# Kernel optimization log

Measured on AMD Instinct MI355X. Metric: run time of the kernel, lower is better.

The kernel has to match this reference:

```python
import jax, jax.numpy as jnp
import numpy as np

# dims: B batch, T frames, N tokens/frame, C embed, H heads, D=C//H, MEM memory slots
B, T, N, C = 8, 16, 196, 768
H = 8
D = C // H
MEM = 196          # mem_size; with N=196 -> _init_t = 1, M stays == MEM
HID = 4 * C        # mlp_ratio * embed_dim
STD = 0.02


def _mlp(x, w1, b1, w2, b2):
    # timm-style Mlp: fc1 -> GELU -> fc2 (dropout = 0)
    return jax.nn.gelu(x @ w1 + b1, approximate=False) @ w2 + b2


def _ln(x, w, b, eps=1e-5):
    mu = jnp.mean(x, axis=-1, keepdims=True)
    var = jnp.var(x, axis=-1, keepdims=True)
    return (x - mu) * jax.lax.rsqrt(var + eps) * w + b


def setup_inputs() -> dict:
    key = jax.random.key(0)
    ks = jax.random.split(key, 10)
    f32 = jnp.float32
    return {
        "cur_fea": jax.random.normal(ks[0], (B, T, N, C), f32),
        "norm1_w": jnp.ones((C,), f32), "norm1_b": jnp.zeros((C,), f32),
        "norm2_w": jnp.ones((C,), f32), "norm2_b": jnp.zeros((C,), f32),
        # c_func: Mlp(2C -> 4C -> C)
        "c_w1": jax.random.normal(ks[1], (2 * C, HID), f32) * STD, "c_b1": jnp.zeros((HID,), f32),
        "c_w2": jax.random.normal(ks[2], (HID, C), f32) * STD, "c_b2": jnp.zeros((C,), f32),
        # m_func: Mlp(C -> 4C -> C)
        "m_w1": jax.random.normal(ks[3], (C, HID), f32) * STD, "m_b1": jnp.zeros((HID,), f32),
        "m_w2": jax.random.normal(ks[4], (HID, C), f32) * STD, "m_b2": jnp.zeros((C,), f32),
        # post_func: Mlp(C -> 4C -> C)
        "p_w1": jax.random.normal(ks[5], (C, HID), f32) * STD, "p_b1": jnp.zeros((HID,), f32),
        "p_w2": jax.random.normal(ks[6], (HID, C), f32) * STD, "p_b2": jnp.zeros((C,), f32),
        # ProjectDotDistance: per-head q(c_global) . k(mem) * scale -> sigmoid
        "q_w": jax.random.normal(ks[7], (C, C), f32) * STD, "q_b": jnp.zeros((C,), f32),
        "k_w": jax.random.normal(ks[8], (C, C), f32) * STD, "k_b": jnp.zeros((C,), f32),
    }


def reference(cur_fea, norm1_w, norm1_b, norm2_w, norm2_b,
              c_w1, c_b1, c_w2, c_b2, m_w1, m_b1, m_w2, m_b2,
              p_w1, p_b1, p_w2, p_b2, q_w, q_b, k_w, k_b):
    x = _ln(cur_fea, norm1_w, norm1_b)                       # [B,T,N,C]
    # T*N > mem_size, _init_t = MEM // N = 1 -> init memory = frame 0 (no grad, torch.no_grad)
    init_mem = jax.lax.stop_gradient(x[:, 0].reshape(B, MEM, C))
    scale = D ** -0.5

    def step(mem, fea):                                      # mem [B,MEM,C], fea [B,N,C]
        ap = jnp.mean(mem, axis=1, keepdims=True)            # [B,1,C]
        cg = _mlp(jnp.concatenate([fea, jnp.broadcast_to(ap, fea.shape)], axis=-1),
                  c_w1, c_b1, c_w2, c_b2)                    # [B,N,C]
        memh = _mlp(mem, m_w1, m_b1, m_w2, m_b2).reshape(B, MEM, H, D).transpose(0, 2, 1, 3)  # [B,H,M,D]
        q = (cg @ q_w + q_b).reshape(B, N, H, D).transpose(0, 2, 1, 3)    # [B,H,N,D]
        k = (mem @ k_w + k_b).reshape(B, MEM, H, D).transpose(0, 2, 1, 3) # [B,H,M,D]
        o = jax.nn.sigmoid(jnp.einsum('bhnd,bhmd->bhnm', q, k) * scale)   # [B,H,N,M]
        cgh = cg.reshape(B, N, H, D).transpose(0, 2, 1, 3)               # [B,H,N,D]
        c = jnp.einsum('bhnm,bhnd->bmhd', o, cgh).reshape(B, MEM, C)
        c = _mlp(c, p_w1, p_b1, p_w2, p_b2)
        # mean_N((1-o) * broadcast(memh)) == mean_N(1-o) * memh (memh indep of N)
        gate = jnp.mean(1.0 - o, axis=2)                     # [B,H,M]
        og = (gate[..., None] * memh).transpose(0, 2, 1, 3).reshape(B, MEM, C)
        new_mem = _ln(c + og, norm2_w, norm2_b)
        return new_mem, None

    fea_seq = x[:, 1:].transpose(1, 0, 2, 3)                 # [T-1,B,N,C]
    final_mem, _ = jax.lax.scan(step, init_mem, fea_seq)
    return final_mem                                         # [B,MEM,C]
```

## Files before the change

### kernel.cpp

```cpp
#include <hip/hip_runtime.h>
#include <hip/hip_bf16.h>
#include <math.h>

constexpr int B_   = 8;
constexpr int T_   = 16;
constexpr int N_   = 196;
constexpr int C_   = 768;
constexpr int H_   = 8;
constexpr int D_   = 96;
constexpr int M_   = 196;
constexpr int HID_ = 3072;
constexpr int ROWS_ = B_ * N_;
constexpr int MP_   = 1664;

typedef __hip_bfloat16 bf16;
typedef __attribute__((ext_vector_type(8))) short bf16x8;
typedef __attribute__((ext_vector_type(4))) float f32x4;

__device__ __forceinline__ float b2f(bf16 x) { return __bfloat162float(x); }
__device__ __forceinline__ short bf2s(bf16 x) { union { bf16 b; short s; } u; u.b = x; return u.s; }
__device__ __forceinline__ float s2f(short x) { union { bf16 b; short s; } u; u.s = x; return __bfloat162float(u.b); }

#define GL2LDS(g, l) __builtin_amdgcn_global_load_lds( \
    (__attribute__((address_space(1))) void*)(g), \
    (__attribute__((address_space(3))) void*)(l), 16, 0, 0)

__device__ __forceinline__ void hard_barrier() {
    asm volatile("" ::: "memory");
    __builtin_amdgcn_s_barrier();
    asm volatile("" ::: "memory");
}

__device__ __forceinline__ float block_reduce_sum256(float v, float* sdata) {
    int tid = threadIdx.x;
    sdata[tid] = v;
    __syncthreads();
    for (int s = 128; s > 0; s >>= 1) {
        if (tid < s) sdata[tid] += sdata[tid + s];
        __syncthreads();
    }
    float r = sdata[0];
    __syncthreads();
    return r;
}

struct TEnt { const float* W; bf16* Wt; int K; int N; int tiles; };
struct TEnts { TEnt e[8]; };

__global__ __launch_bounds__(256) void transpose_all_kernel(TEnts tds)
{
    __shared__ float tile[32][33];
    int local = blockIdx.x;
    int i = 0;
    while (i < 7 && local >= tds.e[i].tiles) { local -= tds.e[i].tiles; ++i; }
    TEnt g = tds.e[i];
    int ntx = g.N / 32;
    int n0 = (local % ntx) * 32, k0 = (local / ntx) * 32;
    int tx = threadIdx.x & 31, ty = threadIdx.x >> 5;
#pragma unroll
    for (int r = 0; r < 32; r += 8)
        tile[ty + r][tx] = g.W[(size_t)(k0 + ty + r) * g.N + n0 + tx];
    __syncthreads();
#pragma unroll
    for (int r = 0; r < 32; r += 8)
        g.Wt[(size_t)(n0 + ty + r) * g.K + k0 + tx] = __float2bfloat16(tile[tx][ty + r]);
}

__global__ __launch_bounds__(256) void cvt_kernel(const float* __restrict__ W,
                                                  bf16* __restrict__ o, int n)
{
    int i = blockIdx.x * 256 + threadIdx.x;
    if (i < n) o[i] = __float2bfloat16(W[i]);
}

__global__ __launch_bounds__(256) void ln_frame_kernel(
    const float* __restrict__ cur, int t,
    const float* __restrict__ w, const float* __restrict__ bia,
    bf16* __restrict__ mem_bf)
{
    __shared__ float sdata[256];
    int row = blockIdx.x;
    int b = row / N_, n = row % N_;
    const float* src = cur + (((size_t)b * T_ + t) * N_ + n) * C_;
    float x[3];
    float sum = 0.f, sumsq = 0.f;
#pragma unroll
    for (int i = 0; i < 3; i++) {
        int c = threadIdx.x + i * 256;
        x[i] = src[c];
        sum += x[i]; sumsq += x[i] * x[i];
    }
    sum = block_reduce_sum256(sum, sdata);
    sumsq = block_reduce_sum256(sumsq, sdata);
    float mu = sum * (1.0f / C_);
    float var = sumsq * (1.0f / C_) - mu * mu;
    float rs = rsqrtf(var + 1e-5f);
#pragma unroll
    for (int i = 0; i < 3; i++) {
        int c = threadIdx.x + i * 256;
        mem_bf[(size_t)row * C_ + c] = __float2bfloat16((x[i] - mu) * rs * w[c] + bia[c]);
    }
}

__global__ __launch_bounds__(768) void ap_kernel(const bf16* __restrict__ mem,
                                                 float* __restrict__ ap)
{
    int b = blockIdx.x;
    int c = threadIdx.x;
    const bf16* p = mem + (size_t)b * M_ * C_ + c;
    float s = 0.f;
    for (int m = 0; m < M_; m++) s += b2f(p[(size_t)m * C_]);
    ap[b * C_ + c] = s * (1.0f / M_);
}

__global__ __launch_bounds__(256) void build_cat_kernel(
    const float* __restrict__ cur, int t,
    const float* __restrict__ w, const float* __restrict__ bia,
    const float* __restrict__ ap, bf16* __restrict__ cat)
{
    __shared__ float sdata[256];
    int row = blockIdx.x;
    int b = row / N_, n = row % N_;
    const float* src = cur + (((size_t)b * T_ + t) * N_ + n) * C_;
    float x[3];
    float sum = 0.f, sumsq = 0.f;
#pragma unroll
    for (int i = 0; i < 3; i++) {
        int c = threadIdx.x + i * 256;
        x[i] = src[c];
        sum += x[i]; sumsq += x[i] * x[i];
    }
    sum = block_reduce_sum256(sum, sdata);
    sumsq = block_reduce_sum256(sumsq, sdata);
    float mu = sum * (1.0f / C_);
    float var = sumsq * (1.0f / C_) - mu * mu;
    float rs = rsqrtf(var + 1e-5f);
    bf16* dstrow = cat + (size_t)row * (2 * C_);
#pragma unroll
    for (int i = 0; i < 3; i++) {
        int c = threadIdx.x + i * 256;
        dstrow[c] = __float2bfloat16((x[i] - mu) * rs * w[c] + bia[c]);
        dstrow[C_ + c] = __float2bfloat16(ap[b * C_ + c]);
    }
}

struct GemmDesc {
    const bf16* A; const bf16* W; const float* bias; bf16* out;
    int K; int N; int ymax; int gelu;
};
struct GemmDescs { GemmDesc d[4]; };

template <int BN>
__global__ __launch_bounds__(256) void mfma_gemm_multi(GemmDescs ds)
{
    constexpr int BM = 128;
    constexpr int TI = 4;
    constexpr int TJ = (BN / 2) / 16;
    constexpr int ABYTES = BM * 128;
    constexpr int BBYTES = BN * 128;
    constexpr int AR = ABYTES / 4096;
    constexpr int BR = BBYTES / 4096;
    constexpr int NL = AR + BR;
    __shared__ short As[2 * BM * 64];
    __shared__ short Bs[2 * BN * 64];

    GemmDesc g = ds.d[blockIdx.z];
    if ((int)blockIdx.y >= g.ymax) return;

    int tid = threadIdx.x;
    int wid = tid >> 6;
    int lane = tid & 63;
    int quad = lane >> 4, l15 = lane & 15;
    int row0 = blockIdx.x * BM;
    int col0 = blockIdx.y * BN;
    int wm = (wid >> 1) * 64;
    int wn = (wid & 1) * (BN / 2);

    f32x4 acc[TI][TJ] = {};

    const char* Ab = (const char*)g.A;
    const char* Wb = (const char*)g.W;
    const size_t Kb = (size_t)g.K * 2;
    const int base = wid * 1024;

    auto stage = [&](int k0, int sel) {
        char* Ad = (char*)As + sel * ABYTES;
        char* Bd = (char*)Bs + sel * BBYTES;
#pragma unroll
        for (int r = 0; r < AR; r++) {
            int o = r * 4096 + base + lane * 16;
            int row = o >> 7, cs = (o >> 4) & 7;
            int kc = cs ^ (row & 7);
            GL2LDS(Ab + (size_t)(row0 + row) * Kb + (size_t)k0 * 2 + kc * 16, Ad + o);
        }
#pragma unroll
        for (int r = 0; r < BR; r++) {
            int o = r * 4096 + base + lane * 16;
            int row = o >> 7, cs = (o >> 4) & 7;
            int kc = cs ^ (row & 7);
            GL2LDS(Wb + (size_t)(col0 + row) * Kb + (size_t)k0 * 2 + kc * 16, Bd + o);
        }
    };

    const int nk = g.K / 64;
    stage(0, 0);
    for (int ki = 0; ki < nk; ki++) {
        int sel = ki & 1;
        if (ki + 1 < nk) {
            stage((ki + 1) * 64, sel ^ 1);
            asm volatile("s_waitcnt vmcnt(%0)" :: "n"(NL) : "memory");
        } else {
            asm volatile("s_waitcnt vmcnt(0)" ::: "memory");
        }
        hard_barrier();
        const bf16x8* Av = (const bf16x8*)(As + sel * BM * 64);
        const bf16x8* Bv = (const bf16x8*)(Bs + sel * BN * 64);
        bf16x8 af[TI][2], bfr[TJ][2];
#pragma unroll
        for (int i = 0; i < TI; i++) {
            int r = wm + i * 16 + l15;
#pragma unroll
            for (int hh = 0; hh < 2; hh++)
                af[i][hh] = Av[r * 8 + ((hh * 4 + quad) ^ (r & 7))];
        }
#pragma unroll
        for (int j = 0; j < TJ; j++) {
            int r = wn + j * 16 + l15;
#pragma unroll
            for (int hh = 0; hh < 2; hh++)
                bfr[j][hh] = Bv[r * 8 + ((hh * 4 + quad) ^ (r & 7))];
        }
#pragma unroll
        for (int hh = 0; hh < 2; hh++)
#pragma unroll
            for (int i = 0; i < TI; i++)
#pragma unroll
                for (int j = 0; j < TJ; j++)
                    acc[i][j] = __builtin_amdgcn_mfma_f32_16x16x32_bf16(
                        af[i][hh], bfr[j][hh], acc[i][j], 0, 0, 0);
        hard_barrier();
    }

#pragma unroll
    for (int i = 0; i < TI; i++) {
        int gr = row0 + wm + i * 16 + quad * 4;
#pragma unroll
        for (int j = 0; j < TJ; j++) {
            int gc = col0 + wn + j * 16 + l15;
            float bv = g.bias ? g.bias[gc] : 0.0f;
#pragma unroll
            for (int r = 0; r < 4; r++) {
                float v = acc[i][j][r] + bv;
                if (g.gelu) v = 0.5f * v * (1.0f + erff(v * 0.7071067811865475f));
                g.out[(size_t)(gr + r) * g.N + gc] = __float2bfloat16(v);
            }
        }
    }
}

__global__ __launch_bounds__(256) void mfma_gemm_splitk(
    const bf16* __restrict__ A, const bf16* __restrict__ Wt,
    float* __restrict__ part, int K)
{
    constexpr int BM = 128;
    constexpr int BN = 64;
    constexpr int TI = 4;
    constexpr int TJ = 2;
    constexpr int ABYTES = BM * 128, BBYTES = BN * 128;
    constexpr int AR = 4, BR = 2, NL = 6;
    __shared__ short As[2 * BM * 64];
    __shared__ short Bs[2 * BN * 64];

    int tid = threadIdx.x;
    int wid = tid >> 6;
    int lane = tid & 63;
    int quad = lane >> 4, l15 = lane & 15;
    int row0 = blockIdx.x * BM;
    int col0 = blockIdx.y * BN;
    int wm = (wid >> 1) * 64;
    int wn = (wid & 1) * 32;
    int kh = K >> 1;
    int kbeg = blockIdx.z * kh;

    f32x4 acc[TI][TJ] = {};
    const char* Ab = (const char*)A;
    const char* Wb = (const char*)Wt;
    const size_t Kb = (size_t)K * 2;
    const int base = wid * 1024;

    auto stage = [&](int k0, int sel) {
        char* Ad = (char*)As + sel * ABYTES;
        char* Bd = (char*)Bs + sel * BBYTES;
#pragma unroll
        for (int r = 0; r < AR; r++) {
            int o = r * 4096 + base + lane * 16;
            int row = o >> 7, cs = (o >> 4) & 7;
            int kc = cs ^ (row & 7);
            GL2LDS(Ab + (size_t)(row0 + row) * Kb + (size_t)k0 * 2 + kc * 16, Ad + o);
        }
#pragma unroll
        for (int r = 0; r < BR; r++) {
            int o = r * 4096 + base + lane * 16;
            int row = o >> 7, cs = (o >> 4) & 7;
            int kc = cs ^ (row & 7);
            GL2LDS(Wb + (size_t)(col0 + row) * Kb + (size_t)k0 * 2 + kc * 16, Bd + o);
        }
    };

    const int nk = kh / 64;
    stage(kbeg, 0);
    for (int ki = 0; ki < nk; ki++) {
        int sel = ki & 1;
        if (ki + 1 < nk) {
            stage(kbeg + (ki + 1) * 64, sel ^ 1);
            asm volatile("s_waitcnt vmcnt(%0)" :: "n"(NL) : "memory");
        } else {
            asm volatile("s_waitcnt vmcnt(0)" ::: "memory");
        }
        hard_barrier();
        const bf16x8* Av = (const bf16x8*)(As + sel * BM * 64);
        const bf16x8* Bv = (const bf16x8*)(Bs + sel * BN * 64);
        bf16x8 af[TI][2], bfr[TJ][2];
#pragma unroll
        for (int i = 0; i < TI; i++) {
            int r = wm + i * 16 + l15;
#pragma unroll
            for (int hh = 0; hh < 2; hh++)
                af[i][hh] = Av[r * 8 + ((hh * 4 + quad) ^ (r & 7))];
        }
#pragma unroll
        for (int j = 0; j < TJ; j++) {
            int r = wn + j * 16 + l15;
#pragma unroll
            for (int hh = 0; hh < 2; hh++)
                bfr[j][hh] = Bv[r * 8 + ((hh * 4 + quad) ^ (r & 7))];
        }
#pragma unroll
        for (int hh = 0; hh < 2; hh++)
#pragma unroll
            for (int i = 0; i < TI; i++)
#pragma unroll
                for (int j = 0; j < TJ; j++)
                    acc[i][j] = __builtin_amdgcn_mfma_f32_16x16x32_bf16(
                        af[i][hh], bfr[j][hh], acc[i][j], 0, 0, 0);
        hard_barrier();
    }

    float* outp = part + (size_t)blockIdx.z * MP_ * C_;
#pragma unroll
    for (int i = 0; i < TI; i++) {
        int gr = row0 + wm + i * 16 + quad * 4;
#pragma unroll
        for (int j = 0; j < TJ; j++) {
            int gc = col0 + wn + j * 16 + l15;
#pragma unroll
            for (int r = 0; r < 4; r++)
                outp[(size_t)(gr + r) * C_ + gc] = acc[i][j][r];
        }
    }
}

__global__ __launch_bounds__(256) void b2q_kernel(
    const float* __restrict__ c_b2, const float* __restrict__ q_b,
    const bf16* __restrict__ W2q_t, float* __restrict__ b2q)
{
    __shared__ float sdata[256];
    int n = blockIdx.x;
    const bf16* row = W2q_t + (size_t)n * HID_;
    float s = 0.f;
    for (int j = threadIdx.x; j < HID_; j += 256) s += c_b2[j] * b2f(row[j]);
    s = block_reduce_sum256(s, sdata);
    if (threadIdx.x == 0) b2q[n] = s + q_b[n];
}

__global__ __launch_bounds__(512) void attn_mfma_kernel(
    const bf16* __restrict__ q, const bf16* __restrict__ k,
    const bf16* __restrict__ cg, bf16* __restrict__ cbuf,
    float* __restrict__ gate)
{
    constexpr int KS = 104;
    constexpr int PSS = 40;
    __shared__ short Ks[64 * KS];
    __shared__ short Qs[32 * KS];
    __shared__ short CGt[96 * PSS];
    __shared__ short Ph[64 * PSS];
    __shared__ short Pl[64 * PSS];
    __shared__ float gred[8][64];

    const int mt = blockIdx.x, h = blockIdx.y, b = blockIdx.z;
    const int m0 = (mt < 3) ? mt * 64 : (M_ - 64);
    const int tid = threadIdx.x;
    const int w = tid >> 6, lane = tid & 63;
    const int quad = lane >> 4, l15 = lane & 15;
    const int wm = w >> 1;
    const int wh = w & 1;
    const float scale = 0.10206207261596575f;

    const bf16* qp = q  + (size_t)b * N_ * C_ + h * D_;
    const bf16* kp = k  + (size_t)b * M_ * C_ + h * D_;
    const bf16* cp = cg + (size_t)b * N_ * C_ + h * D_;

    for (int idx = tid; idx < 64 * 12; idx += 512) {
        int r = idx / 12, c = idx % 12;
        *(bf16x8*)(Ks + r * KS + c * 8) =
            *(const bf16x8*)(kp + (size_t)(m0 + r) * C_ + c * 8);
    }

    f32x4 acc[3] = {};
    float gacc = 0.f;

    const bf16x8 ZEROV = {0, 0, 0, 0, 0, 0, 0, 0};
    bf16x8 qv = ZEROV, cgv = ZEROV;
    const bool active = tid < 32 * 12;
    const int qrow = tid / 12, qcol = (tid % 12) * 8;
    const int cgn = tid & 31, cgd = (tid >> 5) * 8;

    auto issue = [&](int n0) {
        if (!active) return;
        int nq = n0 + qrow;
        qv = (nq < N_) ? *(const bf16x8*)(qp + (size_t)nq * C_ + qcol) : ZEROV;
        int nc = n0 + cgn;
        cgv = (nc < N_) ? *(const bf16x8*)(cp + (size_t)nc * C_ + cgd) : ZEROV;
    };
    auto stage = [&]() {
        if (!active) return;
        *(bf16x8*)(Qs + qrow * KS + qcol) = qv;
#pragma unroll
        for (int i = 0; i < 8; i++) CGt[(cgd + i) * PSS + cgn] = cgv[i];
    };

    issue(0);
    for (int nt = 0; nt < 7; nt++) {
        stage();
        __syncthreads();
        if (nt < 6) issue((nt + 1) * 32);

        f32x4 s4 = {};
#pragma unroll
        for (int kk = 0; kk < 3; kk++) {
            bf16x8 af = *(const bf16x8*)(Ks + (wm * 16 + l15) * KS + kk * 32 + quad * 8);
            bf16x8 bq = *(const bf16x8*)(Qs + (wh * 16 + l15) * KS + kk * 32 + quad * 8);
            s4 = __builtin_amdgcn_mfma_f32_16x16x32_bf16(af, bq, s4, 0, 0, 0);
        }
        const int nglob = nt * 32 + wh * 16 + l15;
#pragma unroll
        for (int r = 0; r < 4; r++) {
            float p = (nglob < N_) ? 1.f / (1.f + expf(-s4[r] * scale)) : 0.f;
            bf16 hb = __float2bfloat16(p);
            bf16 lb = __float2bfloat16(p - __bfloat162float(hb));
            int po = (wm * 16 + quad * 4 + r) * PSS + wh * 16 + l15;
            Ph[po] = bf2s(hb);
            Pl[po] = bf2s(lb);
        }
        __syncthreads();

        {
            const short* ph = Ph + lane * PSS + w * 4;
            const short* pl = Pl + lane * PSS + w * 4;
#pragma unroll
            for (int u = 0; u < 4; u++) gacc += s2f(ph[u]) + s2f(pl[u]);
        }
        bf16x8 pa = *(const bf16x8*)(Ph + (wm * 16 + l15) * PSS + quad * 8);
        bf16x8 pb = *(const bf16x8*)(Pl + (wm * 16 + l15) * PSS + quad * 8);
#pragma unroll
        for (int dt = 0; dt < 3; dt++) {
            bf16x8 bcg = *(const bf16x8*)(CGt + (wh * 48 + dt * 16 + l15) * PSS + quad * 8);
            acc[dt] = __builtin_amdgcn_mfma_f32_16x16x32_bf16(pa, bcg, acc[dt], 0, 0, 0);
            acc[dt] = __builtin_amdgcn_mfma_f32_16x16x32_bf16(pb, bcg, acc[dt], 0, 0, 0);
        }
        __syncthreads();
    }

#pragma unroll
    for (int dt = 0; dt < 3; dt++)
#pragma unroll
        for (int r = 0; r < 4; r++) {
            int m = m0 + wm * 16 + quad * 4 + r;
            cbuf[((size_t)b * M_ + m) * C_ + h * D_ + wh * 48 + dt * 16 + l15] =
                __float2bfloat16(acc[dt][r]);
        }
    gred[w][lane] = gacc;
    __syncthreads();
    if (tid < 64) {
        float g = 0.f;
#pragma unroll
        for (int s = 0; s < 8; s++) g += gred[s][tid];
        gate[((size_t)b * H_ + h) * M_ + m0 + tid] = 1.f - g * (1.0f / N_);
    }
}

__global__ __launch_bounds__(256) void final_kernel(
    const float* __restrict__ part, const float* __restrict__ p_b2,
    const float* __restrict__ gate, const bf16* __restrict__ memh,
    const float* __restrict__ w, const float* __restrict__ bia,
    bf16* __restrict__ mem_bf, float* __restrict__ outp)
{
    __shared__ float sdata[256];
    int row = blockIdx.x;
    int b = row / M_, m = row % M_;
    float x[3];
    float sum = 0.f, sumsq = 0.f;
#pragma unroll
    for (int i = 0; i < 3; i++) {
        int c = threadIdx.x + i * 256;
        int h = c / D_;
        float v = part[(size_t)row * C_ + c] + part[(size_t)MP_ * C_ + (size_t)row * C_ + c]
                + p_b2[c]
                + gate[(b * H_ + h) * M_ + m] * b2f(memh[(size_t)row * C_ + c]);
        x[i] = v;
        sum += v; sumsq += v * v;
    }
    sum = block_reduce_sum256(sum, sdata);
    sumsq = block_reduce_sum256(sumsq, sdata);
    float mu = sum * (1.0f / C_);
    float var = sumsq * (1.0f / C_) - mu * mu;
    float rs = rsqrtf(var + 1e-5f);
#pragma unroll
    for (int i = 0; i < 3; i++) {
        int c = threadIdx.x + i * 256;
        float v = (x[i] - mu) * rs * w[c] + bia[c];
        mem_bf[(size_t)row * C_ + c] = __float2bfloat16(v);
        if (outp) outp[(size_t)row * C_ + c] = v;
    }
}

extern "C" void kernel_launch(void* const* d_in, const int* in_sizes, int n_in,
                              void* d_out, int out_size, void* d_ws, size_t ws_size,
                              hipStream_t stream)
{
    const float* cur_fea = (const float*)d_in[0];
    const float* n1w = (const float*)d_in[1];
    const float* n1b = (const float*)d_in[2];
    const float* n2w = (const float*)d_in[3];
    const float* n2b = (const float*)d_in[4];
    const float* c_w1 = (const float*)d_in[5];
    const float* c_b1 = (const float*)d_in[6];
    const float* c_w2 = (const float*)d_in[7];
    const float* c_b2 = (const float*)d_in[8];
    const float* m_w1 = (const float*)d_in[9];
    const float* m_b1 = (const float*)d_in[10];
    const float* m_w2 = (const float*)d_in[11];
    const float* m_b2 = (const float*)d_in[12];
    const float* p_w1 = (const float*)d_in[13];
    const float* p_b1 = (const float*)d_in[14];
    const float* p_w2 = (const float*)d_in[15];
    const float* p_b2 = (const float*)d_in[16];
    const float* q_w = (const float*)d_in[17];
    const float* q_b = (const float*)d_in[18];
    const float* k_w = (const float*)d_in[19];
    const float* k_b = (const float*)d_in[20];

    size_t off = 0;
    char* base = (char*)d_ws;
    auto carve = [&](size_t bytes) -> char* {
        char* r = base + off;
        off += (bytes + 255) & ~(size_t)255;
        return r;
    };
    bf16* cw1t = (bf16*)carve((size_t)HID_ * (2 * C_) * 2);
    bf16* cw2t = (bf16*)carve((size_t)C_ * HID_ * 2);
    bf16* mw1t = (bf16*)carve((size_t)HID_ * C_ * 2);
    bf16* mw2t = (bf16*)carve((size_t)C_ * HID_ * 2);
    bf16* pw1t = (bf16*)carve((size_t)HID_ * C_ * 2);
    bf16* pw2t = (bf16*)carve((size_t)C_ * HID_ * 2);
    bf16* qwt  = (bf16*)carve((size_t)C_ * C_ * 2);
    bf16* kwt  = (bf16*)carve((size_t)C_ * C_ * 2);
    bf16* mem_bf = (bf16*)carve((size_t)MP_ * C_ * 2);
    char* catreg = carve((size_t)MP_ * 2 * C_ * 2);
    bf16* cat = (bf16*)catreg;
    bf16* qb  = (bf16*)catreg;
    bf16* kb  = (bf16*)catreg + (size_t)MP_ * C_;
    bf16* hid_c = (bf16*)carve((size_t)MP_ * HID_ * 2);
    char* hidm_reg = carve((size_t)MP_ * HID_ * 2);
    bf16*  hid_m = (bf16*)hidm_reg;
    float* part  = (float*)hidm_reg;
    bf16* cg    = (bf16*)carve((size_t)MP_ * C_ * 2);
    bf16* cbuf  = (bf16*)carve((size_t)MP_ * C_ * 2);
    bf16* memh  = (bf16*)carve((size_t)MP_ * C_ * 2);
    float* ap   = (float*)carve((size_t)B_ * C_ * 4);
    float* gateb = (float*)carve((size_t)B_ * H_ * M_ * 4);
    float* b2qb  = (float*)carve((size_t)C_ * 4);
    bf16* W2q_t = (bf16*)carve((size_t)C_ * HID_ * 2);
    const bool fuse_q = (off <= ws_size);

    const dim3 blk(256);

    {
        TEnts tds;
        tds.e[0] = { c_w1, cw1t, 2 * C_, HID_, (HID_ / 32) * ((2 * C_) / 32) };
        tds.e[1] = { c_w2, cw2t, HID_, C_, (C_ / 32) * (HID_ / 32) };
        tds.e[2] = { m_w1, mw1t, C_, HID_, (HID_ / 32) * (C_ / 32) };
        tds.e[3] = { m_w2, mw2t, HID_, C_, (C_ / 32) * (HID_ / 32) };
        tds.e[4] = { p_w1, pw1t, C_, HID_, (HID_ / 32) * (C_ / 32) };
        tds.e[5] = { p_w2, pw2t, HID_, C_, (C_ / 32) * (HID_ / 32) };
        tds.e[6] = { q_w, qwt, C_, C_, (C_ / 32) * (C_ / 32) };
        tds.e[7] = { k_w, kwt, C_, C_, (C_ / 32) * (C_ / 32) };
        int total = 4608 + 2304 * 5 + 576 * 2;
        transpose_all_kernel<<<total, blk, 0, stream>>>(tds);
    }

    if (fuse_q) {
        bf16* cw2nt = hid_c;
        cvt_kernel<<<(HID_ * C_ + 255) / 256, blk, 0, stream>>>(c_w2, cw2nt, HID_ * C_);
        GemmDescs ds;
        ds.d[0] = { qwt, cw2nt, nullptr, W2q_t, C_, HID_, HID_ / 128, 0 };
        ds.d[1] = ds.d[0]; ds.d[2] = ds.d[0]; ds.d[3] = ds.d[0];
        mfma_gemm_multi<128><<<dim3(C_ / 128, HID_ / 128, 1), blk, 0, stream>>>(ds);
        b2q_kernel<<<C_, blk, 0, stream>>>(c_b2, q_b, W2q_t, b2qb);
    }

    ln_frame_kernel<<<ROWS_, blk, 0, stream>>>(cur_fea, 0, n1w, n1b, mem_bf);

    for (int t = 1; t < T_; t++) {
        ap_kernel<<<B_, 768, 0, stream>>>(mem_bf, ap);
        build_cat_kernel<<<ROWS_, blk, 0, stream>>>(cur_fea, t, n1w, n1b, ap, cat);

        {
            GemmDescs ds;
            ds.d[0] = { cat,    cw1t, c_b1, hid_c, 2 * C_, HID_, HID_ / 128, 1 };
            ds.d[1] = { mem_bf, mw1t, m_b1, hid_m, C_,     HID_, HID_ / 128, 1 };
            ds.d[2] = ds.d[0]; ds.d[3] = ds.d[0];
            mfma_gemm_multi<128><<<dim3(MP_ / 128, HID_ / 128, 2), blk, 0, stream>>>(ds);
        }
        {
            GemmDescs ds;
            ds.d[0] = { hid_c,  cw2t, c_b2, cg,   HID_, C_, C_ / 64, 0 };
            ds.d[1] = { hid_m,  mw2t, m_b2, memh, HID_, C_, C_ / 64, 0 };
            ds.d[2] = { mem_bf, kwt,  k_b,  kb,   C_,   C_, C_ / 64, 0 };
            ds.d[3] = { hid_c,  W2q_t, b2qb, qb,  HID_, C_, C_ / 64, 0 };
            mfma_gemm_multi<64><<<dim3(MP_ / 128, C_ / 64, fuse_q ? 4 : 3), blk, 0, stream>>>(ds);
        }
        if (!fuse_q) {
            GemmDescs ds;
            ds.d[0] = { cg, qwt, q_b, qb, C_, C_, C_ / 64, 0 };
            ds.d[1] = ds.d[0]; ds.d[2] = ds.d[0]; ds.d[3] = ds.d[0];
            mfma_gemm_multi<64><<<dim3(MP_ / 128, C_ / 64, 1), blk, 0, stream>>>(ds);
        }
        attn_mfma_kernel<<<dim3(4, H_, B_), dim3(512), 0, stream>>>(qb, kb, cg, cbuf, gateb);
        {
            GemmDescs ds;
            ds.d[0] = { cbuf, pw1t, p_b1, hid_c, C_, HID_, HID_ / 64, 1 };
            ds.d[1] = ds.d[0]; ds.d[2] = ds.d[0]; ds.d[3] = ds.d[0];
            mfma_gemm_multi<64><<<dim3(MP_ / 128, HID_ / 64, 1), blk, 0, stream>>>(ds);
        }
        mfma_gemm_splitk<<<dim3(MP_ / 128, C_ / 64, 2), blk, 0, stream>>>(hid_c, pw2t, part, HID_);
        final_kernel<<<ROWS_, blk, 0, stream>>>(part, p_b2, gateb, memh, n2w, n2b,
                                                mem_bf, (t == T_ - 1) ? (float*)d_out : nullptr);
    }
}
```

Baseline: 2.936 ms.

## Remap workgroups across XCDs for L2 locality and split memory-mean reduction

Adds an XCD-aware block index remapping to the GEMM, split-K and attention kernels so that consecutive logical tiles land on the same XCD and share its L2 cache. The average-pool over memory slots previously ran as 8 blocks, each walking all 196 rows serially. It now runs as 64 blocks that each write a partial sum over 25 rows, and build_cat sums the 8 partials. The remap adds integer index arithmetic to every block, and the partial sums add a small buffer and extra reads in build_cat.

```diff
diff --git a/kernel.cpp b/kernel.cpp
--- a/kernel.cpp
+++ b/kernel.cpp
@@ -31,6 +31,22 @@
     asm volatile("" ::: "memory");
 }
 
+__device__ __forceinline__ int3 xcd_map() {
+    const int gx = gridDim.x, gy = gridDim.y;
+    const int nwg = gx * gy * gridDim.z;
+    const int lid = blockIdx.x + gx * (blockIdx.y + gy * blockIdx.z);
+    const int q = nwg >> 3, r = nwg & 7;
+    const int xcd = lid & 7, pos = lid >> 3;
+    const int wg = (xcd < r) ? (xcd * (q + 1) + pos)
+                             : (r * (q + 1) + (xcd - r) * q + pos);
+    int3 c;
+    c.x = wg % gx;
+    int t = wg / gx;
+    c.y = t % gy;
+    c.z = t / gy;
+    return c;
+}
+
 __device__ __forceinline__ float block_reduce_sum256(float v, float* sdata) {
     int tid = threadIdx.x;
     sdata[tid] = v;
@@ -102,21 +118,26 @@
     }
 }
 
-__global__ __launch_bounds__(768) void ap_kernel(const bf16* __restrict__ mem,
-                                                 float* __restrict__ ap)
-{
-    int b = blockIdx.x;
-    int c = threadIdx.x;
-    const bf16* p = mem + (size_t)b * M_ * C_ + c;
-    float s = 0.f;
-    for (int m = 0; m < M_; m++) s += b2f(p[(size_t)m * C_]);
-    ap[b * C_ + c] = s * (1.0f / M_);
+__global__ __launch_bounds__(256) void ap_partial_kernel(const bf16* __restrict__ mem,
+                                                         float* __restrict__ app)
+{
+    int ch = blockIdx.x, b = blockIdx.y;
+    int m0 = ch * 25;
+    int m1 = m0 + 25; if (m1 > M_) m1 = M_;
+    const bf16* p = mem + (size_t)b * M_ * C_;
+#pragma unroll
+    for (int i = 0; i < 3; i++) {
+        int c = threadIdx.x + i * 256;
+        float s = 0.f;
+        for (int m = m0; m < m1; m++) s += b2f(p[(size_t)m * C_ + c]);
+        app[((size_t)b * 8 + ch) * C_ + c] = s;
+    }
 }
 
 __global__ __launch_bounds__(256) void build_cat_kernel(
     const float* __restrict__ cur, int t,
     const float* __restrict__ w, const float* __restrict__ bia,
-    const float* __restrict__ ap, bf16* __restrict__ cat)
+    const float* __restrict__ app, bf16* __restrict__ cat)
 {
     __shared__ float sdata[256];
     int row = blockIdx.x;
@@ -140,7 +161,10 @@
     for (int i = 0; i < 3; i++) {
         int c = threadIdx.x + i * 256;
         dstrow[c] = __float2bfloat16((x[i] - mu) * rs * w[c] + bia[c]);
-        dstrow[C_ + c] = __float2bfloat16(ap[b * C_ + c]);
+        float apv = 0.f;
+#pragma unroll
+        for (int j = 0; j < 8; j++) apv += app[((size_t)b * 8 + j) * C_ + c];
+        dstrow[C_ + c] = __float2bfloat16(apv * (1.0f / M_));
     }
 }
 
@@ -164,15 +188,16 @@
     __shared__ short As[2 * BM * 64];
     __shared__ short Bs[2 * BN * 64];
 
-    GemmDesc g = ds.d[blockIdx.z];
-    if ((int)blockIdx.y >= g.ymax) return;
+    const int3 bc = xcd_map();
+    GemmDesc g = ds.d[bc.z];
+    if (bc.y >= g.ymax) return;
 
     int tid = threadIdx.x;
     int wid = tid >> 6;
     int lane = tid & 63;
     int quad = lane >> 4, l15 = lane & 15;
-    int row0 = blockIdx.x * BM;
-    int col0 = blockIdx.y * BN;
+    int row0 = bc.x * BM;
+    int col0 = bc.y * BN;
     int wm = (wid >> 1) * 64;
     int wn = (wid & 1) * (BN / 2);
 
@@ -271,16 +296,17 @@
     __shared__ short As[2 * BM * 64];
     __shared__ short Bs[2 * BN * 64];
 
+    const int3 bc = xcd_map();
     int tid = threadIdx.x;
     int wid = tid >> 6;
     int lane = tid & 63;
     int quad = lane >> 4, l15 = lane & 15;
-    int row0 = blockIdx.x * BM;
-    int col0 = blockIdx.y * BN;
+    int row0 = bc.x * BM;
+    int col0 = bc.y * BN;
     int wm = (wid >> 1) * 64;
     int wn = (wid & 1) * 32;
     int kh = K >> 1;
-    int kbeg = blockIdx.z * kh;
+    int kbeg = bc.z * kh;
 
     f32x4 acc[TI][TJ] = {};
     const char* Ab = (const char*)A;
@@ -346,7 +372,7 @@
         hard_barrier();
     }
 
-    float* outp = part + (size_t)blockIdx.z * MP_ * C_;
+    float* outp = part + (size_t)bc.z * MP_ * C_;
 #pragma unroll
     for (int i = 0; i < TI; i++) {
         int gr = row0 + wm + i * 16 + quad * 4;
@@ -387,7 +413,8 @@
     __shared__ short Pl[64 * PSS];
     __shared__ float gred[8][64];
 
-    const int mt = blockIdx.x, h = blockIdx.y, b = blockIdx.z;
+    const int3 bc = xcd_map();
+    const int mt = bc.x, h = bc.y, b = bc.z;
     const int m0 = (mt < 3) ? mt * 64 : (M_ - 64);
     const int tid = threadIdx.x;
     const int w = tid >> 6, lane = tid & 63;
@@ -577,7 +604,7 @@
     bf16* cg    = (bf16*)carve((size_t)MP_ * C_ * 2);
     bf16* cbuf  = (bf16*)carve((size_t)MP_ * C_ * 2);
     bf16* memh  = (bf16*)carve((size_t)MP_ * C_ * 2);
-    float* ap   = (float*)carve((size_t)B_ * C_ * 4);
+    float* ap   = (float*)carve((size_t)B_ * 8 * C_ * 4);
     float* gateb = (float*)carve((size_t)B_ * H_ * M_ * 4);
     float* b2qb  = (float*)carve((size_t)C_ * 4);
     bf16* W2q_t = (bf16*)carve((size_t)C_ * HID_ * 2);
@@ -612,7 +639,7 @@
     ln_frame_kernel<<<ROWS_, blk, 0, stream>>>(cur_fea, 0, n1w, n1b, mem_bf);
 
     for (int t = 1; t < T_; t++) {
-        ap_kernel<<<B_, 768, 0, stream>>>(mem_bf, ap);
+        ap_partial_kernel<<<dim3(8, B_), blk, 0, stream>>>(mem_bf, ap);
         build_cat_kernel<<<ROWS_, blk, 0, stream>>>(cur_fea, t, n1w, n1b, ap, cat);
 
         {
```

New measurement: 3.162 ms. 1.08x slower.

## Split memory average into partial sums and drop GEMM double buffering

Applied to the files above, without the earlier changes.

The per-batch memory column average now runs as an 8x8 grid of partial-sum blocks, each covering 25 memory rows, and build_cat adds up the eight partials. This raises parallelism over the old 8-block reduction. Separately, both MFMA GEMM kernels drop LDS double buffering and instead load, wait and compute each K tile in turn. That halves LDS use, which may raise occupancy, but global loads no longer overlap with MFMA compute.

```diff
diff --git a/kernel.cpp b/kernel.cpp
--- a/kernel.cpp
+++ b/kernel.cpp
@@ -31,6 +31,7 @@
     asm volatile("" ::: "memory");
 }
 
+
 __device__ __forceinline__ float block_reduce_sum256(float v, float* sdata) {
     int tid = threadIdx.x;
     sdata[tid] = v;
@@ -102,21 +103,26 @@
     }
 }
 
-__global__ __launch_bounds__(768) void ap_kernel(const bf16* __restrict__ mem,
-                                                 float* __restrict__ ap)
-{
-    int b = blockIdx.x;
-    int c = threadIdx.x;
-    const bf16* p = mem + (size_t)b * M_ * C_ + c;
-    float s = 0.f;
-    for (int m = 0; m < M_; m++) s += b2f(p[(size_t)m * C_]);
-    ap[b * C_ + c] = s * (1.0f / M_);
+__global__ __launch_bounds__(256) void ap_partial_kernel(const bf16* __restrict__ mem,
+                                                         float* __restrict__ app)
+{
+    int ch = blockIdx.x, b = blockIdx.y;
+    int m0 = ch * 25;
+    int m1 = m0 + 25; if (m1 > M_) m1 = M_;
+    const bf16* p = mem + (size_t)b * M_ * C_;
+#pragma unroll
+    for (int i = 0; i < 3; i++) {
+        int c = threadIdx.x + i * 256;
+        float s = 0.f;
+        for (int m = m0; m < m1; m++) s += b2f(p[(size_t)m * C_ + c]);
+        app[((size_t)b * 8 + ch) * C_ + c] = s;
+    }
 }
 
 __global__ __launch_bounds__(256) void build_cat_kernel(
     const float* __restrict__ cur, int t,
     const float* __restrict__ w, const float* __restrict__ bia,
-    const float* __restrict__ ap, bf16* __restrict__ cat)
+    const float* __restrict__ app, bf16* __restrict__ cat)
 {
     __shared__ float sdata[256];
     int row = blockIdx.x;
@@ -140,7 +146,10 @@
     for (int i = 0; i < 3; i++) {
         int c = threadIdx.x + i * 256;
         dstrow[c] = __float2bfloat16((x[i] - mu) * rs * w[c] + bia[c]);
-        dstrow[C_ + c] = __float2bfloat16(ap[b * C_ + c]);
+        float apv = 0.f;
+#pragma unroll
+        for (int j = 0; j < 8; j++) apv += app[((size_t)b * 8 + j) * C_ + c];
+        dstrow[C_ + c] = __float2bfloat16(apv * (1.0f / M_));
     }
 }
 
@@ -160,9 +169,8 @@
     constexpr int BBYTES = BN * 128;
     constexpr int AR = ABYTES / 4096;
     constexpr int BR = BBYTES / 4096;
-    constexpr int NL = AR + BR;
-    __shared__ short As[2 * BM * 64];
-    __shared__ short Bs[2 * BN * 64];
+    __shared__ short As[BM * 64];
+    __shared__ short Bs[BN * 64];
 
     GemmDesc g = ds.d[blockIdx.z];
     if ((int)blockIdx.y >= g.ymax) return;
@@ -183,9 +191,9 @@
     const size_t Kb = (size_t)g.K * 2;
     const int base = wid * 1024;
 
-    auto stage = [&](int k0, int sel) {
-        char* Ad = (char*)As + sel * ABYTES;
-        char* Bd = (char*)Bs + sel * BBYTES;
+    auto stage = [&](int k0) {
+        char* Ad = (char*)As;
+        char* Bd = (char*)Bs;
 #pragma unroll
         for (int r = 0; r < AR; r++) {
             int o = r * 4096 + base + lane * 16;
@@ -203,18 +211,12 @@
     };
 
     const int nk = g.K / 64;
-    stage(0, 0);
     for (int ki = 0; ki < nk; ki++) {
-        int sel = ki & 1;
-        if (ki + 1 < nk) {
-            stage((ki + 1) * 64, sel ^ 1);
-            asm volatile("s_waitcnt vmcnt(%0)" :: "n"(NL) : "memory");
-        } else {
-            asm volatile("s_waitcnt vmcnt(0)" ::: "memory");
-        }
+        stage(ki * 64);
+        asm volatile("s_waitcnt vmcnt(0)" ::: "memory");
         hard_barrier();
-        const bf16x8* Av = (const bf16x8*)(As + sel * BM * 64);
-        const bf16x8* Bv = (const bf16x8*)(Bs + sel * BN * 64);
+        const bf16x8* Av = (const bf16x8*)As;
+        const bf16x8* Bv = (const bf16x8*)Bs;
         bf16x8 af[TI][2], bfr[TJ][2];
 #pragma unroll
         for (int i = 0; i < TI; i++) {
@@ -266,10 +268,9 @@
     constexpr int BN = 64;
     constexpr int TI = 4;
     constexpr int TJ = 2;
-    constexpr int ABYTES = BM * 128, BBYTES = BN * 128;
-    constexpr int AR = 4, BR = 2, NL = 6;
-    __shared__ short As[2 * BM * 64];
-    __shared__ short Bs[2 * BN * 64];
+    constexpr int AR = 4, BR = 2;
+    __shared__ short As[BM * 64];
+    __shared__ short Bs[BN * 64];
 
     int tid = threadIdx.x;
     int wid = tid >> 6;
@@ -288,9 +289,9 @@
     const size_t Kb = (size_t)K * 2;
     const int base = wid * 1024;
 
-    auto stage = [&](int k0, int sel) {
-        char* Ad = (char*)As + sel * ABYTES;
-        char* Bd = (char*)Bs + sel * BBYTES;
+    auto stage = [&](int k0) {
+        char* Ad = (char*)As;
+        char* Bd = (char*)Bs;
 #pragma unroll
         for (int r = 0; r < AR; r++) {
             int o = r * 4096 + base + lane * 16;
@@ -308,18 +309,12 @@
     };
 
     const int nk = kh / 64;
-    stage(kbeg, 0);
     for (int ki = 0; ki < nk; ki++) {
-        int sel = ki & 1;
-        if (ki + 1 < nk) {
-            stage(kbeg + (ki + 1) * 64, sel ^ 1);
-            asm volatile("s_waitcnt vmcnt(%0)" :: "n"(NL) : "memory");
-        } else {
-            asm volatile("s_waitcnt vmcnt(0)" ::: "memory");
-        }
+        stage(kbeg + ki * 64);
+        asm volatile("s_waitcnt vmcnt(0)" ::: "memory");
         hard_barrier();
-        const bf16x8* Av = (const bf16x8*)(As + sel * BM * 64);
-        const bf16x8* Bv = (const bf16x8*)(Bs + sel * BN * 64);
+        const bf16x8* Av = (const bf16x8*)As;
+        const bf16x8* Bv = (const bf16x8*)Bs;
         bf16x8 af[TI][2], bfr[TJ][2];
 #pragma unroll
         for (int i = 0; i < TI; i++) {
@@ -577,7 +572,7 @@
     bf16* cg    = (bf16*)carve((size_t)MP_ * C_ * 2);
     bf16* cbuf  = (bf16*)carve((size_t)MP_ * C_ * 2);
     bf16* memh  = (bf16*)carve((size_t)MP_ * C_ * 2);
-    float* ap   = (float*)carve((size_t)B_ * C_ * 4);
+    float* app  = (float*)carve((size_t)B_ * 8 * C_ * 4);
     float* gateb = (float*)carve((size_t)B_ * H_ * M_ * 4);
     float* b2qb  = (float*)carve((size_t)C_ * 4);
     bf16* W2q_t = (bf16*)carve((size_t)C_ * HID_ * 2);
@@ -612,8 +607,8 @@
     ln_frame_kernel<<<ROWS_, blk, 0, stream>>>(cur_fea, 0, n1w, n1b, mem_bf);
 
     for (int t = 1; t < T_; t++) {
-        ap_kernel<<<B_, 768, 0, stream>>>(mem_bf, ap);
-        build_cat_kernel<<<ROWS_, blk, 0, stream>>>(cur_fea, t, n1w, n1b, ap, cat);
+        ap_partial_kernel<<<dim3(8, B_), blk, 0, stream>>>(mem_bf, app);
+        build_cat_kernel<<<ROWS_, blk, 0, stream>>>(cur_fea, t, n1w, n1b, app, cat);
 
         {
             GemmDescs ds;
```

Result: slower. 3.090 ms (+5.2%).

## Use 8-wave GEMM blocks, narrower N tiles for fc1, and parallel memory averaging

Applied to the files above, without the earlier changes.

The GEMM kernels move from 4 waves to 8 waves per block, each wave computing a 32-row slice instead of 64, and each wave issuing half as many async loads per stage. The fc1 and W2q GEMMs drop from 128-wide to 64-wide N tiles, which doubles their block count. The single-block-per-batch memory-average kernel is replaced by an 8-way chunked partial sum that build_cat finishes. The aim is more parallelism and latency hiding. The cost is lower per-wave MFMA reuse and extra block scheduling overhead.

```diff
diff --git a/kernel.cpp b/kernel.cpp
--- a/kernel.cpp
+++ b/kernel.cpp
@@ -31,6 +31,7 @@
     asm volatile("" ::: "memory");
 }
 
+
 __device__ __forceinline__ float block_reduce_sum256(float v, float* sdata) {
     int tid = threadIdx.x;
     sdata[tid] = v;
@@ -76,7 +77,7 @@
 __global__ __launch_bounds__(256) void ln_frame_kernel(
     const float* __restrict__ cur, int t,
     const float* __restrict__ w, const float* __restrict__ bia,
-    bf16* __restrict__ mem_bf)
+    bf16* __restrict__ dst)
 {
     __shared__ float sdata[256];
     int row = blockIdx.x;
@@ -98,25 +99,30 @@
 #pragma unroll
     for (int i = 0; i < 3; i++) {
         int c = threadIdx.x + i * 256;
-        mem_bf[(size_t)row * C_ + c] = __float2bfloat16((x[i] - mu) * rs * w[c] + bia[c]);
-    }
-}
-
-__global__ __launch_bounds__(768) void ap_kernel(const bf16* __restrict__ mem,
-                                                 float* __restrict__ ap)
-{
-    int b = blockIdx.x;
-    int c = threadIdx.x;
-    const bf16* p = mem + (size_t)b * M_ * C_ + c;
-    float s = 0.f;
-    for (int m = 0; m < M_; m++) s += b2f(p[(size_t)m * C_]);
-    ap[b * C_ + c] = s * (1.0f / M_);
+        dst[(size_t)row * C_ + c] = __float2bfloat16((x[i] - mu) * rs * w[c] + bia[c]);
+    }
+}
+
+__global__ __launch_bounds__(256) void ap_partial_kernel(const bf16* __restrict__ mem,
+                                                         float* __restrict__ app)
+{
+    int ch = blockIdx.x, b = blockIdx.y;
+    int m0 = ch * 25;
+    int m1 = m0 + 25; if (m1 > M_) m1 = M_;
+    const bf16* p = mem + (size_t)b * M_ * C_;
+#pragma unroll
+    for (int i = 0; i < 3; i++) {
+        int c = threadIdx.x + i * 256;
+        float s = 0.f;
+        for (int m = m0; m < m1; m++) s += b2f(p[(size_t)m * C_ + c]);
+        app[((size_t)b * 8 + ch) * C_ + c] = s;
+    }
 }
 
 __global__ __launch_bounds__(256) void build_cat_kernel(
     const float* __restrict__ cur, int t,
     const float* __restrict__ w, const float* __restrict__ bia,
-    const float* __restrict__ ap, bf16* __restrict__ cat)
+    const float* __restrict__ app, bf16* __restrict__ cat)
 {
     __shared__ float sdata[256];
     int row = blockIdx.x;
@@ -140,7 +146,10 @@
     for (int i = 0; i < 3; i++) {
         int c = threadIdx.x + i * 256;
         dstrow[c] = __float2bfloat16((x[i] - mu) * rs * w[c] + bia[c]);
-        dstrow[C_ + c] = __float2bfloat16(ap[b * C_ + c]);
+        float apv = 0.f;
+#pragma unroll
+        for (int j = 0; j < 8; j++) apv += app[((size_t)b * 8 + j) * C_ + c];
+        dstrow[C_ + c] = __float2bfloat16(apv * (1.0f / M_));
     }
 }
 
@@ -151,15 +160,15 @@
 struct GemmDescs { GemmDesc d[4]; };
 
 template <int BN>
-__global__ __launch_bounds__(256) void mfma_gemm_multi(GemmDescs ds)
+__global__ __launch_bounds__(512) void mfma_gemm_multi(GemmDescs ds)
 {
     constexpr int BM = 128;
-    constexpr int TI = 4;
+    constexpr int TI = 2;
     constexpr int TJ = (BN / 2) / 16;
     constexpr int ABYTES = BM * 128;
     constexpr int BBYTES = BN * 128;
-    constexpr int AR = ABYTES / 4096;
-    constexpr int BR = BBYTES / 4096;
+    constexpr int AR = ABYTES / 8192;
+    constexpr int BR = BBYTES / 8192;
     constexpr int NL = AR + BR;
     __shared__ short As[2 * BM * 64];
     __shared__ short Bs[2 * BN * 64];
@@ -173,7 +182,7 @@
     int quad = lane >> 4, l15 = lane & 15;
     int row0 = blockIdx.x * BM;
     int col0 = blockIdx.y * BN;
-    int wm = (wid >> 1) * 64;
+    int wm = (wid >> 1) * 32;
     int wn = (wid & 1) * (BN / 2);
 
     f32x4 acc[TI][TJ] = {};
@@ -188,14 +197,14 @@
         char* Bd = (char*)Bs + sel * BBYTES;
 #pragma unroll
         for (int r = 0; r < AR; r++) {
-            int o = r * 4096 + base + lane * 16;
+            int o = r * 8192 + base + lane * 16;
             int row = o >> 7, cs = (o >> 4) & 7;
             int kc = cs ^ (row & 7);
             GL2LDS(Ab + (size_t)(row0 + row) * Kb + (size_t)k0 * 2 + kc * 16, Ad + o);
         }
 #pragma unroll
         for (int r = 0; r < BR; r++) {
-            int o = r * 4096 + base + lane * 16;
+            int o = r * 8192 + base + lane * 16;
             int row = o >> 7, cs = (o >> 4) & 7;
             int kc = cs ^ (row & 7);
             GL2LDS(Wb + (size_t)(col0 + row) * Kb + (size_t)k0 * 2 + kc * 16, Bd + o);
@@ -258,16 +267,16 @@
     }
 }
 
-__global__ __launch_bounds__(256) void mfma_gemm_splitk(
+__global__ __launch_bounds__(512) void mfma_gemm_splitk(
     const bf16* __restrict__ A, const bf16* __restrict__ Wt,
     float* __restrict__ part, int K)
 {
     constexpr int BM = 128;
     constexpr int BN = 64;
-    constexpr int TI = 4;
+    constexpr int TI = 2;
     constexpr int TJ = 2;
     constexpr int ABYTES = BM * 128, BBYTES = BN * 128;
-    constexpr int AR = 4, BR = 2, NL = 6;
+    constexpr int AR = 2, BR = 1, NL = 3;
     __shared__ short As[2 * BM * 64];
     __shared__ short Bs[2 * BN * 64];
 
@@ -277,7 +286,7 @@
     int quad = lane >> 4, l15 = lane & 15;
     int row0 = blockIdx.x * BM;
     int col0 = blockIdx.y * BN;
-    int wm = (wid >> 1) * 64;
+    int wm = (wid >> 1) * 32;
     int wn = (wid & 1) * 32;
     int kh = K >> 1;
     int kbeg = blockIdx.z * kh;
@@ -293,14 +302,14 @@
         char* Bd = (char*)Bs + sel * BBYTES;
 #pragma unroll
         for (int r = 0; r < AR; r++) {
-            int o = r * 4096 + base + lane * 16;
+            int o = r * 8192 + base + lane * 16;
             int row = o >> 7, cs = (o >> 4) & 7;
             int kc = cs ^ (row & 7);
             GL2LDS(Ab + (size_t)(row0 + row) * Kb + (size_t)k0 * 2 + kc * 16, Ad + o);
         }
 #pragma unroll
         for (int r = 0; r < BR; r++) {
-            int o = r * 4096 + base + lane * 16;
+            int o = r * 8192 + base + lane * 16;
             int row = o >> 7, cs = (o >> 4) & 7;
             int kc = cs ^ (row & 7);
             GL2LDS(Wb + (size_t)(col0 + row) * Kb + (size_t)k0 * 2 + kc * 16, Bd + o);
@@ -577,13 +586,14 @@
     bf16* cg    = (bf16*)carve((size_t)MP_ * C_ * 2);
     bf16* cbuf  = (bf16*)carve((size_t)MP_ * C_ * 2);
     bf16* memh  = (bf16*)carve((size_t)MP_ * C_ * 2);
-    float* ap   = (float*)carve((size_t)B_ * C_ * 4);
+    float* app  = (float*)carve((size_t)B_ * 8 * C_ * 4);
     float* gateb = (float*)carve((size_t)B_ * H_ * M_ * 4);
     float* b2qb  = (float*)carve((size_t)C_ * 4);
     bf16* W2q_t = (bf16*)carve((size_t)C_ * HID_ * 2);
     const bool fuse_q = (off <= ws_size);
 
     const dim3 blk(256);
+    const dim3 blk512(512);
 
     {
         TEnts tds;
@@ -603,24 +613,24 @@
         bf16* cw2nt = hid_c;
         cvt_kernel<<<(HID_ * C_ + 255) / 256, blk, 0, stream>>>(c_w2, cw2nt, HID_ * C_);
         GemmDescs ds;
-        ds.d[0] = { qwt, cw2nt, nullptr, W2q_t, C_, HID_, HID_ / 128, 0 };
+        ds.d[0] = { qwt, cw2nt, nullptr, W2q_t, C_, HID_, HID_ / 64, 0 };
         ds.d[1] = ds.d[0]; ds.d[2] = ds.d[0]; ds.d[3] = ds.d[0];
-        mfma_gemm_multi<128><<<dim3(C_ / 128, HID_ / 128, 1), blk, 0, stream>>>(ds);
+        mfma_gemm_multi<64><<<dim3(C_ / 128, HID_ / 64, 1), blk512, 0, stream>>>(ds);
         b2q_kernel<<<C_, blk, 0, stream>>>(c_b2, q_b, W2q_t, b2qb);
     }
 
     ln_frame_kernel<<<ROWS_, blk, 0, stream>>>(cur_fea, 0, n1w, n1b, mem_bf);
 
     for (int t = 1; t < T_; t++) {
-        ap_kernel<<<B_, 768, 0, stream>>>(mem_bf, ap);
-        build_cat_kernel<<<ROWS_, blk, 0, stream>>>(cur_fea, t, n1w, n1b, ap, cat);
+        ap_partial_kernel<<<dim3(8, B_), blk, 0, stream>>>(mem_bf, app);
+        build_cat_kernel<<<ROWS_, blk, 0, stream>>>(cur_fea, t, n1w, n1b, app, cat);
 
         {
             GemmDescs ds;
-            ds.d[0] = { cat,    cw1t, c_b1, hid_c, 2 * C_, HID_, HID_ / 128, 1 };
-            ds.d[1] = { mem_bf, mw1t, m_b1, hid_m, C_,     HID_, HID_ / 128, 1 };
+            ds.d[0] = { cat,    cw1t, c_b1, hid_c, 2 * C_, HID_, HID_ / 64, 1 };
+            ds.d[1] = { mem_bf, mw1t, m_b1, hid_m, C_,     HID_, HID_ / 64, 1 };
             ds.d[2] = ds.d[0]; ds.d[3] = ds.d[0];
-            mfma_gemm_multi<128><<<dim3(MP_ / 128, HID_ / 128, 2), blk, 0, stream>>>(ds);
+            mfma_gemm_multi<64><<<dim3(MP_ / 128, HID_ / 64, 2), blk512, 0, stream>>>(ds);
         }
         {
             GemmDescs ds;
@@ -628,22 +638,22 @@
             ds.d[1] = { hid_m,  mw2t, m_b2, memh, HID_, C_, C_ / 64, 0 };
             ds.d[2] = { mem_bf, kwt,  k_b,  kb,   C_,   C_, C_ / 64, 0 };
             ds.d[3] = { hid_c,  W2q_t, b2qb, qb,  HID_, C_, C_ / 64, 0 };
-            mfma_gemm_multi<64><<<dim3(MP_ / 128, C_ / 64, fuse_q ? 4 : 3), blk, 0, stream>>>(ds);
+            mfma_gemm_multi<64><<<dim3(MP_ / 128, C_ / 64, fuse_q ? 4 : 3), blk512, 0, stream>>>(ds);
         }
         if (!fuse_q) {
             GemmDescs ds;
             ds.d[0] = { cg, qwt, q_b, qb, C_, C_, C_ / 64, 0 };
             ds.d[1] = ds.d[0]; ds.d[2] = ds.d[0]; ds.d[3] = ds.d[0];
-            mfma_gemm_multi<64><<<dim3(MP_ / 128, C_ / 64, 1), blk, 0, stream>>>(ds);
+            mfma_gemm_multi<64><<<dim3(MP_ / 128, C_ / 64, 1), blk512, 0, stream>>>(ds);
         }
         attn_mfma_kernel<<<dim3(4, H_, B_), dim3(512), 0, stream>>>(qb, kb, cg, cbuf, gateb);
         {
             GemmDescs ds;
             ds.d[0] = { cbuf, pw1t, p_b1, hid_c, C_, HID_, HID_ / 64, 1 };
             ds.d[1] = ds.d[0]; ds.d[2] = ds.d[0]; ds.d[3] = ds.d[0];
-            mfma_gemm_multi<64><<<dim3(MP_ / 128, HID_ / 64, 1), blk, 0, stream>>>(ds);
-        }
-        mfma_gemm_splitk<<<dim3(MP_ / 128, C_ / 64, 2), blk, 0, stream>>>(hid_c, pw2t, part, HID_);
+            mfma_gemm_multi<64><<<dim3(MP_ / 128, HID_ / 64, 1), blk512, 0, stream>>>(ds);
+        }
+        mfma_gemm_splitk<<<dim3(MP_ / 128, C_ / 64, 2), blk512, 0, stream>>>(hid_c, pw2t, part, HID_);
         final_kernel<<<ROWS_, blk, 0, stream>>>(part, p_b2, gateb, memh, n2w, n2b,
                                                 mem_bf, (t == T_ - 1) ? (float*)d_out : nullptr);
     }
```

Measured after the change: 3.053 ms. 4.0% more time.
